# Performance work log

Measured on AMD Instinct MI355X. Metric: run time of the kernel, lower is better.

## Reference

```python
import jax, jax.numpy as jnp
import numpy as np

HIDDEN = 4096
NUM_HEADS = 32
NUM_KV_HEADS = 8
HEAD_DIM = HIDDEN // NUM_HEADS  # 128
Q_SIZE = NUM_HEADS * HEAD_DIM    # 4096
KV_SIZE = NUM_KV_HEADS * HEAD_DIM  # 1024
SCALE = 1.0 / HEAD_DIM  # attention_multiplier=None -> head_dim ** (-1)
ROPE_BASE = 10000.0


def _rope_neox(x, positions):
    # x: [B, S, H, D], positions: [B, S] int
    half = HEAD_DIM // 2
    inv_freq = 1.0 / (ROPE_BASE ** (jnp.arange(0, half, dtype=jnp.float32) / half))
    freqs = positions.astype(jnp.float32)[..., None] * inv_freq  # [B, S, half]
    cos = jnp.cos(freqs)[:, :, None, :]  # [B, S, 1, half]
    sin = jnp.sin(freqs)[:, :, None, :]
    x1, x2 = x[..., :half], x[..., half:]
    return jnp.concatenate([x1 * cos - x2 * sin, x2 * cos + x1 * sin], axis=-1)


def setup_inputs() -> dict:
    key = jax.random.key(0)
    k1, k2, k3 = jax.random.split(key, 3)
    B, S = 2, 2048
    positions = jnp.broadcast_to(jnp.arange(S, dtype=jnp.int32), (B, S))
    hidden_states = jax.random.normal(k1, (B, S, HIDDEN), dtype=jnp.float32) * 0.02
    w_qkv = jax.random.normal(k2, (Q_SIZE + 2 * KV_SIZE, HIDDEN), dtype=jnp.float32) * 0.02
    w_o = jax.random.normal(k3, (HIDDEN, Q_SIZE), dtype=jnp.float32) * 0.02
    return {"positions": positions, "hidden_states": hidden_states, "w_qkv": w_qkv, "w_o": w_o}


def reference(positions, hidden_states, w_qkv, w_o):
    B, S, _ = hidden_states.shape
    # fused QKV projection
    qkv = jnp.einsum('bsh,oh->bso', hidden_states, w_qkv)
    q = qkv[..., :Q_SIZE].reshape(B, S, NUM_HEADS, HEAD_DIM)
    k = qkv[..., Q_SIZE:Q_SIZE + KV_SIZE].reshape(B, S, NUM_KV_HEADS, HEAD_DIM)
    v = qkv[..., Q_SIZE + KV_SIZE:].reshape(B, S, NUM_KV_HEADS, HEAD_DIM)
    # neox-style RoPE on q and k
    q = _rope_neox(q, positions)
    k = _rope_neox(k, positions)
    # GQA: repeat kv heads
    rep = NUM_HEADS // NUM_KV_HEADS
    k = jnp.repeat(k, rep, axis=2)  # [B, S, NUM_HEADS, D]
    v = jnp.repeat(v, rep, axis=2)
    # causal attention
    scores = jnp.einsum('bqhd,bkhd->bhqk', q, k) * SCALE
    causal = jnp.tril(jnp.ones((S, S), dtype=bool))
    scores = jnp.where(causal, scores, jnp.finfo(scores.dtype).min)
    probs = jax.nn.softmax(scores, axis=-1)
    attn = jnp.einsum('bhqk,bkhd->bqhd', probs, v).reshape(B, S, Q_SIZE)
    # output projection
    return jnp.einsum('bsq,hq->bsh', attn, w_o)
```

## Files before the change

kernel.cpp:

```cpp
#include <hip/hip_runtime.h>
#include <hip/hip_bf16.h>
#include <cmath>

typedef __bf16 bf16x8 __attribute__((ext_vector_type(8)));
typedef __bf16 bf16x4 __attribute__((ext_vector_type(4)));
typedef float  f32x4  __attribute__((ext_vector_type(4)));
typedef unsigned int u32;
typedef u32 u32x4 __attribute__((ext_vector_type(4)));

#define AS1 __attribute__((address_space(1)))
#define AS3 __attribute__((address_space(3)))
#define GLDS16(gp, lp) __builtin_amdgcn_global_load_lds((AS1 void*)(gp), (AS3 void*)(lp), 16, 0, 0)

#define B_DIM 2
#define S_LEN 2048
#define HIDDEN 4096
#define NHEADS 32
#define NKV 8
#define HDIM 128
#define QSZ 4096
#define KVSZ 1024
#define QKVSZ 6144
#define GK 4096
#define ATT_SCALE 0.0078125f
#define L2E 1.4426950408889634f

__global__ __launch_bounds__(256) void conv3_f32_bf16(const float* __restrict__ i0, __bf16* __restrict__ o0, int n0,
                                                      const float* __restrict__ i1, __bf16* __restrict__ o1, int n1,
                                                      const float* __restrict__ i2, __bf16* __restrict__ o2, int n2) {
    const int total = n0 + n1 + n2;
    for (int idx = blockIdx.x * 256 + threadIdx.x; idx < total; idx += gridDim.x * 256) {
        const float* in; __bf16* out; int j = idx;
        if (j < n0) { in = i0; out = o0; }
        else if ((j -= n0) < n1) { in = i1; out = o1; }
        else { j -= n1; in = i2; out = o2; }
        float4 v = ((const float4*)in)[j];
        bf16x4 o;
        o[0] = (__bf16)v.x; o[1] = (__bf16)v.y; o[2] = (__bf16)v.z; o[3] = (__bf16)v.w;
        ((bf16x4*)out)[j] = o;
    }
}

__global__ __launch_bounds__(256) void rope_table_kernel(float* __restrict__ ct,
                                                         float* __restrict__ st) {
    int idx = blockIdx.x * 256 + threadIdx.x;
    int p = idx >> 6, i = idx & 63;
    float inv = expf(-(float)i * (9.210340371976184f / 64.0f));
    float freq = (float)p * inv;
    float s, c;
    sincosf(freq, &s, &c);
    ct[idx] = c; st[idx] = s;
}

template<typename OUT>
__global__ __launch_bounds__(512, 2) void gemm256(const __bf16* __restrict__ A,
                                                  const __bf16* __restrict__ B,
                                                  OUT* __restrict__ C,
                                                  int N) {
    __shared__ __bf16 Asm[2 * 16384 + 2 * 16384];
    char* Bbase = (char*)Asm + 65536;

    const int tid = threadIdx.x;
    const int w = tid >> 6, l = tid & 63;
    const int l15 = l & 15, l4 = l >> 4;
    const int wr = w >> 2, wc = w & 3;

    const int nwg = gridDim.x * gridDim.y;
    const int orig = blockIdx.y * gridDim.x + blockIdx.x;
    const int swz = (orig & 7) * (nwg >> 3) + (orig >> 3);
    const int bx = swz % gridDim.x, by = swz / gridDim.x;
    const int m0 = by * 256, n0 = bx * 256;

    const __bf16* Ag = A + (size_t)m0 * GK;
    const __bf16* Bg = B + (size_t)n0 * GK;

#define STAGE_AQ(q, tile) do {                                                  \
        int c_ = (q) * 512 + tid;                                               \
        int r_ = c_ >> 3;                                                       \
        int jg_ = (tid & 7) ^ (r_ & 7);                                         \
        GLDS16(Ag + (size_t)r_ * GK + (tile) * 64 + jg_ * 8,                    \
               (char*)Asm + ((tile) & 1) * 32768 + c_ * 16);                    \
    } while (0)
#define STAGE_BS(s, tile) do {                                                  \
        _Pragma("unroll")                                                       \
        for (int i_ = 0; i_ < 2; ++i_) {                                        \
            int v_ = i_ * 512 + tid;                                            \
            int r_ = (v_ >> 8) * 64 + (s) * 32 + ((v_ >> 3) & 31);              \
            int jg_ = (v_ & 7) ^ (r_ & 7);                                      \
            int c_ = r_ * 8 + (v_ & 7);                                         \
            GLDS16(Bg + (size_t)r_ * GK + (tile) * 64 + jg_ * 8,                \
                   Bbase + ((tile) & 1) * 32768 + c_ * 16);                     \
        }                                                                       \
    } while (0)

#define LOAD_A(DST, MH) do {                                                    \
        _Pragma("unroll")                                                       \
        for (int m2 = 0; m2 < 4; ++m2) {                                        \
            int row = wr * 128 + ((MH) * 4 + m2) * 16 + l15;                    \
            _Pragma("unroll")                                                   \
            for (int kk = 0; kk < 2; ++kk) {                                    \
                int j = (kk * 4 + l4) ^ (row & 7);                              \
                DST[m2][kk] = *(const bf16x8*)(Als + row * 64 + j * 8);         \
            }                                                                   \
        }                                                                       \
    } while (0)
#define LOAD_B(DST, NH) do {                                                    \
        _Pragma("unroll")                                                       \
        for (int n2 = 0; n2 < 2; ++n2) {                                        \
            int row = wc * 64 + ((NH) * 2 + n2) * 16 + l15;                     \
            _Pragma("unroll")                                                   \
            for (int kk = 0; kk < 2; ++kk) {                                    \
                int j = (kk * 4 + l4) ^ (row & 7);                              \
                DST[n2][kk] = *(const bf16x8*)(Bls + row * 64 + j * 8);         \
            }                                                                   \
        }                                                                       \
    } while (0)
#define MFMA_QUAD(AF, BF, MI0, NI0)                                             \
    _Pragma("unroll")                                                           \
    for (int m2 = 0; m2 < 4; ++m2)                                              \
        _Pragma("unroll")                                                       \
        for (int n2 = 0; n2 < 2; ++n2)                                          \
            _Pragma("unroll")                                                   \
            for (int kk = 0; kk < 2; ++kk)                                      \
                acc[(MI0) + m2][(NI0) + n2] =                                   \
                    __builtin_amdgcn_mfma_f32_16x16x32_bf16(                    \
                        AF[m2][kk], BF[n2][kk], acc[(MI0) + m2][(NI0) + n2], 0, 0, 0);

    f32x4 acc[8][4] = {};

    const int T = GK / 64;
    STAGE_AQ(0, 0); STAGE_AQ(1, 0); STAGE_AQ(2, 0); STAGE_AQ(3, 0);
    STAGE_BS(0, 0); STAGE_BS(1, 0);
    STAGE_AQ(0, 1); STAGE_AQ(2, 1); STAGE_BS(0, 1);
    asm volatile("s_waitcnt vmcnt(4)" ::: "memory");
    __builtin_amdgcn_s_barrier();

    for (int t = 0; t < T; ++t) {
        const __bf16* Als = Asm + (t & 1) * 16384;
        const __bf16* Bls = (__bf16*)Bbase + (t & 1) * 16384;
        bf16x8 af0[4][2], af1[4][2], bfr[2][2];
        LOAD_A(af0, 0);
        LOAD_B(bfr, 0);
        if (t + 1 < T) { STAGE_AQ(1, t + 1); STAGE_AQ(3, t + 1); }
        __builtin_amdgcn_s_barrier();
        __builtin_amdgcn_s_setprio(1);
        MFMA_QUAD(af0, bfr, 0, 0);
        __builtin_amdgcn_s_setprio(0);
        __builtin_amdgcn_s_barrier();
        LOAD_B(bfr, 1);
        if (t + 1 < T) STAGE_BS(1, t + 1);
        __builtin_amdgcn_s_barrier();
        __builtin_amdgcn_s_setprio(1);
        MFMA_QUAD(af0, bfr, 0, 2);
        __builtin_amdgcn_s_setprio(0);
        __builtin_amdgcn_s_barrier();
        LOAD_A(af1, 1);
        LOAD_B(bfr, 0);
        if (t + 2 < T) { STAGE_AQ(0, t + 2); STAGE_AQ(2, t + 2); }
        __builtin_amdgcn_s_barrier();
        __builtin_amdgcn_s_setprio(1);
        MFMA_QUAD(af1, bfr, 4, 0);
        __builtin_amdgcn_s_setprio(0);
        __builtin_amdgcn_s_barrier();
        LOAD_B(bfr, 1);
        if (t + 2 < T) STAGE_BS(0, t + 2);
        __builtin_amdgcn_s_barrier();
        __builtin_amdgcn_s_setprio(1);
        MFMA_QUAD(af1, bfr, 4, 2);
        __builtin_amdgcn_s_setprio(0);
        if (t + 2 < T)      { asm volatile("s_waitcnt vmcnt(4)" ::: "memory"); }
        else if (t + 1 < T) { asm volatile("s_waitcnt vmcnt(0)" ::: "memory"); }
        __builtin_amdgcn_s_barrier();
    }
#undef MFMA_QUAD
#undef LOAD_A
#undef LOAD_B
#undef STAGE_AQ
#undef STAGE_BS

#pragma unroll
    for (int mi = 0; mi < 8; ++mi)
#pragma unroll
        for (int ni = 0; ni < 4; ++ni)
#pragma unroll
            for (int r = 0; r < 4; ++r)
                C[(size_t)(m0 + wr * 128 + mi * 16 + l4 * 4 + r) * N
                  + n0 + wc * 64 + ni * 16 + l15] = (OUT)acc[mi][ni][r];
}

__global__ __launch_bounds__(256) void rope_kernel(const __bf16* __restrict__ qkv,
                                                   const int* __restrict__ pos,
                                                   const float* __restrict__ ct,
                                                   const float* __restrict__ st,
                                                   __bf16* __restrict__ Qb,
                                                   __bf16* __restrict__ Kb) {
    const int tid = threadIdx.x;
    const int tok = blockIdx.x;
    const int b = tok >> 11, s = tok & 2047;
    const int p = pos[tok];
    const __bf16* base = qkv + (size_t)tok * QKVSZ;
    const float* cb = ct + (size_t)p * 64;
    const float* sb = st + (size_t)p * 64;
    for (int idx = tid; idx < 2560; idx += 256) {
        int head = idx >> 6, i = idx & 63;
        float c = cb[i], sn = sb[i];
        if (head < 32) {
            float x1 = (float)base[head * HDIM + i];
            float x2 = (float)base[head * HDIM + 64 + i];
            size_t o = ((size_t)(b * 32 + head) * S_LEN + s) * HDIM + i;
            Qb[o]      = (__bf16)((x1 * c - x2 * sn) * ATT_SCALE);
            Qb[o + 64] = (__bf16)((x2 * c + x1 * sn) * ATT_SCALE);
        } else {
            int g = head - 32;
            float x1 = (float)base[QSZ + g * HDIM + i];
            float x2 = (float)base[QSZ + g * HDIM + 64 + i];
            size_t o = ((size_t)(b * 8 + g) * S_LEN + s) * HDIM + i;
            Kb[o]      = (__bf16)(x1 * c - x2 * sn);
            Kb[o + 64] = (__bf16)(x2 * c + x1 * sn);
        }
    }
}

__global__ __launch_bounds__(256) void vtrans_kernel(const __bf16* __restrict__ qkv,
                                                     __bf16* __restrict__ Vt) {
    __shared__ __bf16 T[64][132];
    const int tid = threadIdx.x;
    const int st = blockIdx.x, g = blockIdx.y, b = blockIdx.z;
    const __bf16* src = qkv + ((size_t)(b * S_LEN + st * 64)) * QKVSZ + (QSZ + KVSZ) + g * HDIM;
#pragma unroll
    for (int it = 0; it < 8; ++it) {
        int c = it * 256 + tid;
        int row = c >> 5;
        int c4 = c & 31;
        bf16x4 v = *(const bf16x4*)(src + (size_t)row * QKVSZ + c4 * 4);
        *(bf16x4*)(&T[row][c4 * 4]) = v;
    }
    __syncthreads();
#pragma unroll
    for (int it = 0; it < 8; ++it) {
        int c = it * 256 + tid;
        int d = c >> 4;
        int s4 = (c & 15) * 4;
        bf16x4 o;
        o[0] = T[s4 + 0][d]; o[1] = T[s4 + 1][d]; o[2] = T[s4 + 2][d]; o[3] = T[s4 + 3][d];
        *(bf16x4*)(Vt + ((size_t)(b * 8 + g) * HDIM + d) * S_LEN + st * 64 + s4) = o;
    }
}

__global__ __launch_bounds__(512, 2) void attn_kernel(const __bf16* __restrict__ Q,
                                                      const __bf16* __restrict__ K,
                                                      const __bf16* __restrict__ Vt,
                                                      __bf16* __restrict__ O) {
    const int tid = threadIdx.x;
    const int w = tid >> 6, l = tid & 63;
    const int l15 = l & 15, l4 = l >> 4;
    const int flat = blockIdx.x + (blockIdx.y << 2) + (blockIdx.z << 7);
    const int swz = (flat & 7) * 32 + (flat >> 3);
    const int p = swz & 3;
    const int hb = swz >> 2;
    const int h = hb & 31, b = hb >> 5;
    const int g = h >> 2;

    __shared__ __bf16 Ks[4][64 * 128];
    __shared__ __bf16 Vs[4][128 * 64];

    const __bf16* Kp = K + (size_t)(b * 8 + g) * S_LEN * HDIM;
    const __bf16* Vp = Vt + (size_t)(b * 8 + g) * HDIM * S_LEN;

#define RED16(x, OPINS) do {                                                      \
        u32 ra_ = __builtin_bit_cast(u32, x), rb_;                                \
        asm("v_mov_b32 %0, %1" : "=v"(rb_) : "v"(ra_));                           \
        asm("v_permlane16_swap_b32 %0, %1" : "+v"(ra_), "+v"(rb_));               \
        x = OPINS(__builtin_bit_cast(float, ra_), __builtin_bit_cast(float, rb_));\
    } while (0)
#define RED32(x, OPINS) do {                                                      \
        u32 ra_ = __builtin_bit_cast(u32, x), rb_;                                \
        asm("v_mov_b32 %0, %1" : "=v"(rb_) : "v"(ra_));                           \
        asm("v_permlane32_swap_b32 %0, %1" : "+v"(ra_), "+v"(rb_));               \
        x = OPINS(__builtin_bit_cast(float, ra_), __builtin_bit_cast(float, rb_));\
    } while (0)
#define FADD_(a_, b_) ((a_) + (b_))

#define STAGE(ktile) do {                                                          \
        const int buf_ = (ktile) & 3;                                              \
        const __bf16* kbase = Kp + (size_t)(ktile) * 64 * HDIM;                    \
        _Pragma("unroll")                                                          \
        for (int i_ = 0; i_ < 2; ++i_) {                                           \
            int c_ = i_ * 512 + tid;                \
            int row_ = c_ >> 4, cc_ = (c_ & 15) ^ (row_ & 7);                      \
            GLDS16(kbase + (size_t)row_ * HDIM + cc_ * 8,                          \
                   (char*)Ks[buf_] + c_ * 16);                                     \
        }                                                                          \
        const __bf16* vbase = Vp + (size_t)(ktile) * 64;                           \
        _Pragma("unroll")                                                          \
        for (int i_ = 0; i_ < 2; ++i_) {                                           \
            int c_ = i_ * 512 + tid;                \
            int row_ = c_ >> 3, cc_ = (c_ & 7) ^ (row_ & 7);                       \
            GLDS16(vbase + (size_t)row_ * S_LEN + cc_ * 8,                         \
                   (char*)Vs[buf_] + c_ * 16);                                     \
        }                                                                          \
    } while (0)

    for (int pi = 0; pi < 2; ++pi) {
        const int qt = pi ? (7 - p) : p;
        const int qw0 = qt * 256 + w * 32;
        const __bf16* Qp = Q + ((size_t)((b * 32 + h) * S_LEN + qw0)) * HDIM;

        bf16x8 qf[2][4];
#pragma unroll
        for (int qh = 0; qh < 2; ++qh)
#pragma unroll
            for (int kk = 0; kk < 4; ++kk)
                qf[qh][kk] = *(const bf16x8*)(Qp + (size_t)(qh * 16 + l15) * HDIM + kk * 32 + l4 * 8);

        f32x4 acc[2][8] = {};
        float m[2]    = {-1e30f, -1e30f};
        float lsum[2] = {0.f, 0.f};

        const int nkt = 4 * qt + 4;
        if (pi) { asm volatile("s_waitcnt vmcnt(0)" ::: "memory"); }
        STAGE(0);
        STAGE(1);
        STAGE(2);

        for (int kt = 0; kt < nkt; ++kt) {
            if (kt + 3 < nkt) STAGE(kt + 3);
            {
                int rem = nkt - 1 - kt;
                if (rem >= 3)      { asm volatile("s_waitcnt vmcnt(12)" ::: "memory"); }
                else if (rem == 2) { asm volatile("s_waitcnt vmcnt(8)"  ::: "memory"); }
                else if (rem == 1) { asm volatile("s_waitcnt vmcnt(4)"  ::: "memory"); }
                else               { asm volatile("s_waitcnt vmcnt(0)"  ::: "memory"); }
            }
            __builtin_amdgcn_sched_barrier(0);
            __builtin_amdgcn_s_barrier();
            __builtin_amdgcn_sched_barrier(0);
            const int cur = kt & 3;
            if (kt * 64 <= qw0 + 31) {
                f32x4 sfr[2][4];
                __builtin_amdgcn_s_setprio(1);
#pragma unroll
                for (int fn = 0; fn < 4; ++fn) {
                    f32x4 sa0 = {}, sa1 = {};
#pragma unroll
                    for (int kk = 0; kk < 4; ++kk) {
                        int row = fn * 16 + l15;
                        int cc = (kk * 4 + l4) ^ (l15 & 7);
                        bf16x8 kb = *(const bf16x8*)(Ks[cur] + row * HDIM + cc * 8);
                        sa0 = __builtin_amdgcn_mfma_f32_16x16x32_bf16(kb, qf[0][kk], sa0, 0, 0, 0);
                        sa1 = __builtin_amdgcn_mfma_f32_16x16x32_bf16(kb, qf[1][kk], sa1, 0, 0, 0);
                    }
                    sfr[0][fn] = sa0; sfr[1][fn] = sa1;
                }
                __builtin_amdgcn_s_setprio(0);
                const bool needmask = (kt * 64 + 63 > qw0);
                bf16x8 pb[2][2];
#pragma unroll
                for (int qh = 0; qh < 2; ++qh) {
                    const int qrow = qw0 + qh * 16 + l15;
                    float pmax = -1e30f;
#pragma unroll
                    for (int fn = 0; fn < 4; ++fn)
#pragma unroll
                        for (int r = 0; r < 4; ++r) {
                            float v = sfr[qh][fn][r];
                            if (needmask) {
                                int kcol = kt * 64 + fn * 16 + l4 * 4 + r;
                                if (kcol > qrow) v = -1e30f;
                            }
                            sfr[qh][fn][r] = v;
                            pmax = fmaxf(pmax, v);
                        }
                    RED16(pmax, fmaxf);
                    RED32(pmax, fmaxf);
                    if (!__all(pmax - m[qh] <= 8.0f)) {
                        float mn = fmaxf(m[qh], pmax);
                        float alpha = exp2f((m[qh] - mn) * L2E);
                        m[qh] = mn;
                        lsum[qh] *= alpha;
#pragma unroll
                        for (int n = 0; n < 8; ++n)
#pragma unroll
                            for (int r = 0; r < 4; ++r) acc[qh][n][r] *= alpha;
                    }
                    float rs = 0.f;
                    u32 pk01[4], pk23[4];
#pragma unroll
                    for (int fn = 0; fn < 4; ++fn) {
                        float p0 = exp2f((sfr[qh][fn][0] - m[qh]) * L2E);
                        float p1 = exp2f((sfr[qh][fn][1] - m[qh]) * L2E);
                        float p2 = exp2f((sfr[qh][fn][2] - m[qh]) * L2E);
                        float p3 = exp2f((sfr[qh][fn][3] - m[qh]) * L2E);
                        rs += (p0 + p1) + (p2 + p3);
                        asm("v_cvt_pk_bf16_f32 %0, %1, %2" : "=v"(pk01[fn]) : "v"(p0), "v"(p1));
                        asm("v_cvt_pk_bf16_f32 %0, %1, %2" : "=v"(pk23[fn]) : "v"(p2), "v"(p3));
                    }
                    RED16(rs, FADD_);
                    RED32(rs, FADD_);
                    lsum[qh] += rs;
#pragma unroll
                    for (int kk = 0; kk < 2; ++kk) {
                        u32 w0 = pk01[2 * kk], w2 = pk01[2 * kk + 1];
                        asm("v_permlane32_swap_b32 %0, %1" : "+v"(w0), "+v"(w2));
                        asm("v_permlane16_swap_b32 %0, %1" : "+v"(w0), "+v"(w2));
                        u32 w1 = pk23[2 * kk], w3 = pk23[2 * kk + 1];
                        asm("v_permlane32_swap_b32 %0, %1" : "+v"(w1), "+v"(w3));
                        asm("v_permlane16_swap_b32 %0, %1" : "+v"(w1), "+v"(w3));
                        u32x4 wv;
                        wv[0] = w0; wv[1] = w1; wv[2] = w2; wv[3] = w3;
                        pb[qh][kk] = __builtin_bit_cast(bf16x8, wv);
                    }
                }
                __builtin_amdgcn_s_setprio(1);
#pragma unroll
                for (int kk = 0; kk < 2; ++kk) {
#pragma unroll
                    for (int n = 0; n < 8; ++n) {
                        int row = n * 16 + l15;
                        int cc = (kk * 4 + l4) ^ (l15 & 7);
                        bf16x8 vb = *(const bf16x8*)(Vs[cur] + row * 64 + cc * 8);
                        acc[0][n] = __builtin_amdgcn_mfma_f32_16x16x32_bf16(vb, pb[0][kk], acc[0][n], 0, 0, 0);
                        acc[1][n] = __builtin_amdgcn_mfma_f32_16x16x32_bf16(vb, pb[1][kk], acc[1][n], 0, 0, 0);
                    }
                }
                __builtin_amdgcn_s_setprio(0);
            }
            __builtin_amdgcn_sched_barrier(0);
            __builtin_amdgcn_s_barrier();
            __builtin_amdgcn_sched_barrier(0);
        }
#pragma unroll
        for (int qh = 0; qh < 2; ++qh) {
            float inv = 1.0f / lsum[qh];
            int qrow = qw0 + qh * 16 + l15;
            __bf16* obase = O + ((size_t)(b * S_LEN) + qrow) * QSZ + h * HDIM + l4 * 4;
#pragma unroll
            for (int n = 0; n < 8; ++n) {
                bf16x4 o4;
#pragma unroll
                for (int r = 0; r < 4; ++r) o4[r] = (__bf16)(acc[qh][n][r] * inv);
                *(bf16x4*)(obase + n * 16) = o4;
            }
        }
    }
#undef STAGE
#undef RED16
#undef RED32
#undef FADD_
}

extern "C" void kernel_launch(void* const* d_in, const int* in_sizes, int n_in,
                              void* d_out, int out_size, void* d_ws, size_t ws_size,
                              hipStream_t stream) {
    const int*   pos    = (const int*)d_in[0];
    const float* hidden = (const float*)d_in[1];
    const float* wqkv   = (const float*)d_in[2];
    const float* wo     = (const float*)d_in[3];
    float* out = (float*)d_out;

    __bf16* hb    = (__bf16*)d_ws;
    __bf16* wqb   = hb  + 16777216;
    __bf16* wob   = wqb + 25165824;
    __bf16* qkv   = wob + 16777216;
    __bf16* Qb    = qkv + 25165824;
    __bf16* Kb    = Qb  + 16777216;
    __bf16* Vtb   = Kb  + 4194304;
    __bf16* attnb = Vtb + 4194304;
    float*  rc    = (float*)(attnb + 16777216);
    float*  rs    = rc + 131072;

    conv3_f32_bf16<<<2048, 256, 0, stream>>>(hidden, hb, 4194304,
                                             wqkv, wqb, 6291456,
                                             wo, wob, 4194304);
    rope_table_kernel<<<512, 256, 0, stream>>>(rc, rs);
    gemm256<__bf16><<<dim3(QKVSZ / 256, (B_DIM * S_LEN) / 256), 512, 0, stream>>>(hb, wqb, qkv, QKVSZ);
    rope_kernel<<<B_DIM * S_LEN, 256, 0, stream>>>(qkv, pos, rc, rs, Qb, Kb);
    vtrans_kernel<<<dim3(S_LEN / 64, NKV, B_DIM), 256, 0, stream>>>(qkv, Vtb);
    attn_kernel<<<dim3(4, NHEADS, B_DIM), 512, 0, stream>>>(Qb, Kb, Vtb, attnb);
    gemm256<float><<<dim3(HIDDEN / 256, (B_DIM * S_LEN) / 256), 512, 0, stream>>>(attnb, wob, out, HIDDEN);
}
```

Baseline: 524.0 us.

## Split-K the QKV projection GEMM into two halves and sum partials downstream

The QKV GEMM grid is 24x16=384 blocks of 256x256 tiles, about 1.5 waves at 2 blocks per CU on 256 CUs. This splits K into two halves along a z grid dimension, doubling the block count to fill the machine more evenly. Each half writes a bf16 partial result, and rope and vtrans read both partials and add them in fp32. The cost is an extra 50MB of partial writes and reads, plus rounding each partial to bf16 before the sum.

```diff
diff --git a/kernel.cpp b/kernel.cpp
--- a/kernel.cpp
+++ b/kernel.cpp
@@ -56,7 +56,7 @@
 __global__ __launch_bounds__(512, 2) void gemm256(const __bf16* __restrict__ A,
                                                   const __bf16* __restrict__ B,
                                                   OUT* __restrict__ C,
-                                                  int N) {
+                                                  int N, int Tloc, size_t zstride) {
     __shared__ __bf16 Asm[2 * 16384 + 2 * 16384];
     char* Bbase = (char*)Asm + 65536;
 
@@ -71,8 +71,10 @@
     const int bx = swz % gridDim.x, by = swz / gridDim.x;
     const int m0 = by * 256, n0 = bx * 256;
 
-    const __bf16* Ag = A + (size_t)m0 * GK;
-    const __bf16* Bg = B + (size_t)n0 * GK;
+    const int kt0 = blockIdx.z * Tloc;
+    const __bf16* Ag = A + (size_t)m0 * GK + (size_t)kt0 * 64;
+    const __bf16* Bg = B + (size_t)n0 * GK + (size_t)kt0 * 64;
+    OUT* Cz = C + (size_t)blockIdx.z * zstride;
 
 #define STAGE_AQ(q, tile) do {                                                  \
         int c_ = (q) * 512 + tid;                                               \
@@ -128,7 +130,7 @@
 
     f32x4 acc[8][4] = {};
 
-    const int T = GK / 64;
+    const int T = Tloc;
     STAGE_AQ(0, 0); STAGE_AQ(1, 0); STAGE_AQ(2, 0); STAGE_AQ(3, 0);
     STAGE_BS(0, 0); STAGE_BS(1, 0);
     STAGE_AQ(0, 1); STAGE_AQ(2, 1); STAGE_BS(0, 1);
@@ -184,11 +186,12 @@
         for (int ni = 0; ni < 4; ++ni)
 #pragma unroll
             for (int r = 0; r < 4; ++r)
-                C[(size_t)(m0 + wr * 128 + mi * 16 + l4 * 4 + r) * N
-                  + n0 + wc * 64 + ni * 16 + l15] = (OUT)acc[mi][ni][r];
-}
-
-__global__ __launch_bounds__(256) void rope_kernel(const __bf16* __restrict__ qkv,
+                Cz[(size_t)(m0 + wr * 128 + mi * 16 + l4 * 4 + r) * N
+                   + n0 + wc * 64 + ni * 16 + l15] = (OUT)acc[mi][ni][r];
+}
+
+__global__ __launch_bounds__(256) void rope_kernel(const __bf16* __restrict__ qkv0,
+                                                   const __bf16* __restrict__ qkv1,
                                                    const int* __restrict__ pos,
                                                    const float* __restrict__ ct,
                                                    const float* __restrict__ st,
@@ -198,22 +201,23 @@
     const int tok = blockIdx.x;
     const int b = tok >> 11, s = tok & 2047;
     const int p = pos[tok];
-    const __bf16* base = qkv + (size_t)tok * QKVSZ;
+    const __bf16* b0 = qkv0 + (size_t)tok * QKVSZ;
+    const __bf16* b1 = qkv1 + (size_t)tok * QKVSZ;
     const float* cb = ct + (size_t)p * 64;
     const float* sb = st + (size_t)p * 64;
     for (int idx = tid; idx < 2560; idx += 256) {
         int head = idx >> 6, i = idx & 63;
         float c = cb[i], sn = sb[i];
         if (head < 32) {
-            float x1 = (float)base[head * HDIM + i];
-            float x2 = (float)base[head * HDIM + 64 + i];
+            float x1 = (float)b0[head * HDIM + i]      + (float)b1[head * HDIM + i];
+            float x2 = (float)b0[head * HDIM + 64 + i] + (float)b1[head * HDIM + 64 + i];
             size_t o = ((size_t)(b * 32 + head) * S_LEN + s) * HDIM + i;
             Qb[o]      = (__bf16)((x1 * c - x2 * sn) * ATT_SCALE);
             Qb[o + 64] = (__bf16)((x2 * c + x1 * sn) * ATT_SCALE);
         } else {
             int g = head - 32;
-            float x1 = (float)base[QSZ + g * HDIM + i];
-            float x2 = (float)base[QSZ + g * HDIM + 64 + i];
+            float x1 = (float)b0[QSZ + g * HDIM + i]      + (float)b1[QSZ + g * HDIM + i];
+            float x2 = (float)b0[QSZ + g * HDIM + 64 + i] + (float)b1[QSZ + g * HDIM + 64 + i];
             size_t o = ((size_t)(b * 8 + g) * S_LEN + s) * HDIM + i;
             Kb[o]      = (__bf16)(x1 * c - x2 * sn);
             Kb[o + 64] = (__bf16)(x2 * c + x1 * sn);
@@ -221,19 +225,26 @@
     }
 }
 
-__global__ __launch_bounds__(256) void vtrans_kernel(const __bf16* __restrict__ qkv,
+__global__ __launch_bounds__(256) void vtrans_kernel(const __bf16* __restrict__ qkv0,
+                                                     const __bf16* __restrict__ qkv1,
                                                      __bf16* __restrict__ Vt) {
     __shared__ __bf16 T[64][132];
     const int tid = threadIdx.x;
     const int st = blockIdx.x, g = blockIdx.y, b = blockIdx.z;
-    const __bf16* src = qkv + ((size_t)(b * S_LEN + st * 64)) * QKVSZ + (QSZ + KVSZ) + g * HDIM;
+    const size_t off = ((size_t)(b * S_LEN + st * 64)) * QKVSZ + (QSZ + KVSZ) + g * HDIM;
+    const __bf16* s0 = qkv0 + off;
+    const __bf16* s1 = qkv1 + off;
 #pragma unroll
     for (int it = 0; it < 8; ++it) {
         int c = it * 256 + tid;
         int row = c >> 5;
         int c4 = c & 31;
-        bf16x4 v = *(const bf16x4*)(src + (size_t)row * QKVSZ + c4 * 4);
-        *(bf16x4*)(&T[row][c4 * 4]) = v;
+        bf16x4 v0 = *(const bf16x4*)(s0 + (size_t)row * QKVSZ + c4 * 4);
+        bf16x4 v1 = *(const bf16x4*)(s1 + (size_t)row * QKVSZ + c4 * 4);
+        bf16x4 o;
+#pragma unroll
+        for (int k = 0; k < 4; ++k) o[k] = (__bf16)((float)v0[k] + (float)v1[k]);
+        *(bf16x4*)(&T[row][c4 * 4]) = o;
     }
     __syncthreads();
 #pragma unroll
@@ -461,8 +472,8 @@
     __bf16* hb    = (__bf16*)d_ws;
     __bf16* wqb   = hb  + 16777216;
     __bf16* wob   = wqb + 25165824;
-    __bf16* qkv   = wob + 16777216;
-    __bf16* Qb    = qkv + 25165824;
+    __bf16* qkvP  = wob + 16777216;
+    __bf16* Qb    = qkvP + 2 * 25165824;
     __bf16* Kb    = Qb  + 16777216;
     __bf16* Vtb   = Kb  + 4194304;
     __bf16* attnb = Vtb + 4194304;
@@ -473,9 +484,11 @@
                                              wqkv, wqb, 6291456,
                                              wo, wob, 4194304);
     rope_table_kernel<<<512, 256, 0, stream>>>(rc, rs);
-    gemm256<__bf16><<<dim3(QKVSZ / 256, (B_DIM * S_LEN) / 256), 512, 0, stream>>>(hb, wqb, qkv, QKVSZ);
-    rope_kernel<<<B_DIM * S_LEN, 256, 0, stream>>>(qkv, pos, rc, rs, Qb, Kb);
-    vtrans_kernel<<<dim3(S_LEN / 64, NKV, B_DIM), 256, 0, stream>>>(qkv, Vtb);
+    gemm256<__bf16><<<dim3(QKVSZ / 256, (B_DIM * S_LEN) / 256, 2), 512, 0, stream>>>(
+        hb, wqb, qkvP, QKVSZ, 32, (size_t)25165824);
+    rope_kernel<<<B_DIM * S_LEN, 256, 0, stream>>>(qkvP, qkvP + 25165824, pos, rc, rs, Qb, Kb);
+    vtrans_kernel<<<dim3(S_LEN / 64, NKV, B_DIM), 256, 0, stream>>>(qkvP, qkvP + 25165824, Vtb);
     attn_kernel<<<dim3(4, NHEADS, B_DIM), 512, 0, stream>>>(Qb, Kb, Vtb, attnb);
-    gemm256<float><<<dim3(HIDDEN / 256, (B_DIM * S_LEN) / 256), 512, 0, stream>>>(attnb, wob, out, HIDDEN);
-}
+    gemm256<float><<<dim3(HIDDEN / 256, (B_DIM * S_LEN) / 256, 1), 512, 0, stream>>>(
+        attnb, wob, out, HIDDEN, 64, (size_t)0);
+}
```

Result: no change. 530.6 us (+1.3%).
